# Kernel optimization log

Measured on AMD Instinct MI355X. Metric: run time of the kernel, lower is better.

The kernel has to match this reference:

```python
import jax, jax.numpy as jnp
import numpy as np

N_JOB, N_SKILL = 100000, 20000
H, D = 4, 64            # heads, per-head dim (hidden_channels)
F_DIM = H * D           # 256 = heads * hidden_channels
IN = 256                # in_channels
E_SJ, E_JJ, E_JS = 500000, 500000, 250000


def setup_inputs() -> dict:
    key = jax.random.key(0)
    ks = jax.random.split(key, 24)
    rn = lambda k, s, sc=0.05: jax.random.normal(k, s, dtype=jnp.float32) * sc
    z = lambda s: jnp.zeros(s, jnp.float32)
    return dict(
        x_job=rn(ks[0], (N_JOB, IN), 1.0),
        x_skill=rn(ks[1], (N_SKILL, IN), 1.0),
        W_job=rn(ks[2], (IN, F_DIM)), b_job=z((F_DIM,)),
        W_skill=rn(ks[3], (IN, F_DIM)), b_skill=z((F_DIM,)),
        a_src_sj=rn(ks[4], (H, D)), a_dst_sj=rn(ks[5], (H, D)),
        a_src_jj=rn(ks[6], (H, D)), a_dst_jj=rn(ks[7], (H, D)),
        a_src_js=rn(ks[8], (H, D)), a_dst_js=rn(ks[9], (H, D)),
        q=rn(ks[10], (F_DIM,)), Wk=rn(ks[11], (F_DIM, F_DIM)), bk=z((F_DIM,)),
        W1=rn(ks[12], (F_DIM, F_DIM)), b1=z((F_DIM,)),
        W2=rn(ks[13], (F_DIM, 1)), b2=z((1,)),
        ei_sj_src=jax.random.randint(ks[14], (E_SJ,), 0, N_SKILL),
        ei_sj_dst=jax.random.randint(ks[15], (E_SJ,), 0, N_JOB),
        ei_jj_src=jax.random.randint(ks[16], (E_JJ,), 0, N_JOB),
        ei_jj_dst=jax.random.randint(ks[17], (E_JJ,), 0, N_JOB),
        ei_js_src=jax.random.randint(ks[18], (E_JS,), 0, N_JOB),
        ei_js_dst=jax.random.randint(ks[19], (E_JS,), 0, N_SKILL),
    )


def _gat(x_src, x_dst, a_src, a_dst, src, dst, n_dst):
    # x_src: [Ns,H,D], x_dst: [Nd,H,D]; GAT-style node-level attention per edge type.
    al = jnp.einsum('nhd,hd->nh', x_src, a_src)[src] + jnp.einsum('nhd,hd->nh', x_dst, a_dst)[dst]
    al = jax.nn.leaky_relu(al, 0.2)                      # [E,H]
    amax = jax.lax.stop_gradient(jax.ops.segment_max(al, dst, n_dst))
    e = jnp.exp(al - amax[dst])
    denom = jax.ops.segment_sum(e, dst, n_dst)
    alpha = e / (denom[dst] + 1e-16)                     # softmax over incoming edges per dst
    out = jax.ops.segment_sum(x_src[src] * alpha[:, :, None], dst, n_dst)  # [Nd,H,D]
    return jax.nn.relu(out.reshape(n_dst, H * D))


def _group(outs, q, Wk, bk):
    # semantic-level attention across edge types (shared q, k_lin)
    stk = jnp.stack(outs)                                # [M,N,F]
    score = jnp.einsum('f,mf->m', q, jnp.tanh(stk @ Wk + bk).mean(1))
    attn = jax.nn.softmax(score)
    return jnp.einsum('m,mnf->nf', attn, stk)


def reference(x_job, x_skill, W_job, b_job, W_skill, b_skill,
              a_src_sj, a_dst_sj, a_src_jj, a_dst_jj, a_src_js, a_dst_js,
              q, Wk, bk, W1, b1, W2, b2,
              ei_sj_src, ei_sj_dst, ei_jj_src, ei_jj_dst, ei_js_src, ei_js_dst):
    h_job = (x_job @ W_job + b_job).reshape(N_JOB, H, D)
    h_skill = (x_skill @ W_skill + b_skill).reshape(N_SKILL, H, D)
    out_sj = _gat(h_skill, h_job, a_src_sj, a_dst_sj, ei_sj_src, ei_sj_dst, N_JOB)
    out_jj = _gat(h_job, h_job, a_src_jj, a_dst_jj, ei_jj_src, ei_jj_dst, N_JOB)
    out_js = _gat(h_job, h_skill, a_src_js, a_dst_js, ei_js_src, ei_js_dst, N_SKILL)
    job = _group([out_sj, out_jj], q, Wk, bk)            # 'job' node type
    _ = _group([out_js], q, Wk, bk)                      # 'skill' node type (unused by head)
    # dropout is identity in eval mode; MLP head (mlp_layers=2)
    h = jax.nn.relu(job @ W1 + b1)
    return (h @ W2 + b2)[:, 0]
```

## Files before the change

### kernel.cpp

```cpp
#include <hip/hip_runtime.h>
#include <hip/hip_bf16.h>
#include <math.h>

#define SCAN_B 256
#define NEG_BIG (-3.0e38f)

typedef __attribute__((ext_vector_type(8))) short bf16x8;
typedef __attribute__((ext_vector_type(4))) float f32x4;

__device__ __forceinline__ unsigned short f2bf(float f) {
    __hip_bfloat16 h = __float2bfloat16(f);
    return *(unsigned short*)&h;
}
__device__ __forceinline__ float bf2f(unsigned short u) {
    unsigned v = ((unsigned)u) << 16;
    return __uint_as_float(v);
}
__device__ __forceinline__ float lrelu(float x) { return (x >= 0.f) ? x : 0.2f * x; }

__device__ __forceinline__ unsigned blend2(unsigned a, unsigned b, float c0, float c1) {
    float alo = bf2f((unsigned short)(a & 0xffff)), ahi = bf2f((unsigned short)(a >> 16));
    float blo = bf2f((unsigned short)(b & 0xffff)), bhi = bf2f((unsigned short)(b >> 16));
    unsigned short rlo = f2bf(c0 * alo + c1 * blo);
    unsigned short rhi = f2bf(c0 * ahi + c1 * bhi);
    return (unsigned)rlo | ((unsigned)rhi << 16);
}

__device__ __forceinline__ void fma8(float* a, uint4 u, float w) {
    a[0] += w * __uint_as_float(u.x << 16);
    a[1] += w * __uint_as_float(u.x & 0xffff0000u);
    a[2] += w * __uint_as_float(u.y << 16);
    a[3] += w * __uint_as_float(u.y & 0xffff0000u);
    a[4] += w * __uint_as_float(u.z << 16);
    a[5] += w * __uint_as_float(u.z & 0xffff0000u);
    a[6] += w * __uint_as_float(u.w << 16);
    a[7] += w * __uint_as_float(u.w & 0xffff0000u);
}

template<int MODE, int NV, int AF32>
__launch_bounds__(512)
__global__ void gemm_mfma(const float* __restrict__ Af32,
                          const unsigned short* __restrict__ Abf,
                          const unsigned short* __restrict__ A2bf,
                          const unsigned short* __restrict__ Bt,
                          const float* __restrict__ bias,
                          const float* __restrict__ vq,
                          const float* __restrict__ b2p,
                          const float* __restrict__ attn2,
                          unsigned short* __restrict__ outh,
                          float* __restrict__ outf,
                          float* __restrict__ scoreSlot,
                          const float* __restrict__ av0,
                          const float* __restrict__ av1,
                          const float* __restrict__ av2,
                          float* __restrict__ lo0,
                          float* __restrict__ lo1,
                          float* __restrict__ lo2,
                          int M)
{
    __shared__ __align__(16) char sm[49152];
    __shared__ float red8[8];
    const int t    = threadIdx.x;
    const int lane = t & 63, wid = t >> 6;
    const int wr = wid >> 2, wc = wid & 3;
    const long row0 = (long)blockIdx.x * 128;
    const char* Ab = (const char*)((MODE == 1 && blockIdx.y == 1) ? A2bf : Abf);
    const char* A2 = (const char*)A2bf;
    const char* Bb = (const char*)Bt;

    float blend0 = 0.f, blend1 = 0.f;
    if (MODE == 2) { blend0 = attn2[0]; blend1 = attn2[1]; }

    f32x4 acc[4][4];
#pragma unroll
    for (int m = 0; m < 4; ++m)
#pragma unroll
        for (int n = 0; n < 4; ++n) acc[m][n] = (f32x4){0.f, 0.f, 0.f, 0.f};

    for (int k0 = 0; k0 < 256; k0 += 64) {
#pragma unroll
        for (int rep = 0; rep < 2; ++rep) {
            int idx = rep * 512 + t;
            int row = idx >> 3, colb = (idx & 7) << 4;
            uint4 v;
            if (AF32) {
                long grow = row0 + row;
                if (grow < M) {
                    const float* sp = Af32 + grow * 256 + k0 + ((idx & 7) << 3);
                    float4 f0 = *(const float4*)sp;
                    float4 f1 = *(const float4*)(sp + 4);
                    v.x = (unsigned)f2bf(f0.x) | ((unsigned)f2bf(f0.y) << 16);
                    v.y = (unsigned)f2bf(f0.z) | ((unsigned)f2bf(f0.w) << 16);
                    v.z = (unsigned)f2bf(f1.x) | ((unsigned)f2bf(f1.y) << 16);
                    v.w = (unsigned)f2bf(f1.z) | ((unsigned)f2bf(f1.w) << 16);
                } else {
                    v = make_uint4(0u, 0u, 0u, 0u);
                }
            } else {
                v = *(const uint4*)(Ab + (row0 + row) * 512 + k0 * 2 + colb);
                if (MODE == 2) {
                    uint4 v2 = *(const uint4*)(A2 + (row0 + row) * 512 + k0 * 2 + colb);
                    v.x = blend2(v.x, v2.x, blend0, blend1);
                    v.y = blend2(v.y, v2.y, blend0, blend1);
                    v.z = blend2(v.z, v2.z, blend0, blend1);
                    v.w = blend2(v.w, v2.w, blend0, blend1);
                }
            }
            *(uint4*)&sm[row * 128 + (colb ^ ((row & 7) << 4))] = v;
        }
#pragma unroll
        for (int rep = 0; rep < 4; ++rep) {
            int idx = rep * 512 + t;
            int n = idx >> 3, colb = (idx & 7) << 4;
            uint4 v = *(const uint4*)(Bb + n * 512 + k0 * 2 + colb);
            *(uint4*)&sm[16384 + n * 128 + (colb ^ ((n & 7) << 4))] = v;
        }
        __syncthreads();
#pragma unroll
        for (int kki = 0; kki < 2; ++kki) {
            const int kb = kki * 64 + ((lane >> 4) << 4);
            bf16x8 a[4], b[4];
#pragma unroll
            for (int m = 0; m < 4; ++m) {
                int row = wr * 64 + m * 16 + (lane & 15);
                a[m] = *(const bf16x8*)&sm[row * 128 + (kb ^ ((row & 7) << 4))];
            }
#pragma unroll
            for (int n = 0; n < 4; ++n) {
                int nr = wc * 64 + n * 16 + (lane & 15);
                b[n] = *(const bf16x8*)&sm[16384 + nr * 128 + (kb ^ ((nr & 7) << 4))];
            }
#pragma unroll
            for (int m = 0; m < 4; ++m)
#pragma unroll
                for (int n = 0; n < 4; ++n)
                    acc[m][n] = __builtin_amdgcn_mfma_f32_16x16x32_bf16(a[m], b[n], acc[m][n], 0, 0, 0);
        }
        __syncthreads();
    }

    const int colbase = wc * 64 + (lane & 15);
    const int rbase   = wr * 64 + ((lane >> 4) << 2);
    float bv[4];
#pragma unroll
    for (int n = 0; n < 4; ++n) bv[n] = bias[colbase + n * 16];

    if (MODE == 0) {
        float areg[(NV > 0) ? NV : 1][4];
#pragma unroll
        for (int v = 0; v < NV; ++v) {
            const float* av = (v == 0) ? av0 : (v == 1) ? av1 : av2;
#pragma unroll
            for (int n = 0; n < 4; ++n) areg[v][n] = av[colbase + n * 16];
        }
#pragma unroll
        for (int m = 0; m < 4; ++m) {
#pragma unroll
            for (int j = 0; j < 4; ++j) {
                long row = row0 + rbase + m * 16 + j;
                float hv[4];
#pragma unroll
                for (int n = 0; n < 4; ++n) hv[n] = acc[m][n][j] + bv[n];
                if (row < M) {
#pragma unroll
                    for (int n = 0; n < 4; ++n)
                        outh[row * 256 + colbase + n * 16] = f2bf(hv[n]);
                }
#pragma unroll
                for (int v = 0; v < NV; ++v) {
                    float p = hv[0] * areg[v][0] + hv[1] * areg[v][1]
                            + hv[2] * areg[v][2] + hv[3] * areg[v][3];
                    p += __shfl_xor(p, 1); p += __shfl_xor(p, 2);
                    p += __shfl_xor(p, 4); p += __shfl_xor(p, 8);
                    if ((lane & 15) == 0 && row < M) {
                        float* lo = (v == 0) ? lo0 : (v == 1) ? lo1 : lo2;
                        lo[row * 4 + wc] = p;
                    }
                }
            }
        }
    } else if (MODE == 1) {
        float p = 0.f;
        float qv[4];
#pragma unroll
        for (int n = 0; n < 4; ++n) qv[n] = vq[colbase + n * 16];
#pragma unroll
        for (int n = 0; n < 4; ++n) {
#pragma unroll
            for (int m = 0; m < 4; ++m) {
                long row = row0 + rbase + m * 16;
#pragma unroll
                for (int j = 0; j < 4; ++j)
                    if (row + j < M) p += qv[n] * tanhf(acc[m][n][j] + bv[n]);
            }
        }
#pragma unroll
        for (int off = 32; off > 0; off >>= 1) p += __shfl_xor(p, off);
        if (lane == 0) red8[wid] = p;
        __syncthreads();
        if (t == 0) {
            float s = 0.f;
#pragma unroll
            for (int i = 0; i < 8; ++i) s += red8[i];
            atomicAdd(&scoreSlot[blockIdx.y], s);
        }
    } else {
        float* redC = (float*)sm;
        float b2v = b2p[0];
        float wv[4];
#pragma unroll
        for (int n = 0; n < 4; ++n) wv[n] = vq[colbase + n * 16];
#pragma unroll
        for (int m = 0; m < 4; ++m) {
#pragma unroll
            for (int j = 0; j < 4; ++j) {
                float s = 0.f;
#pragma unroll
                for (int n = 0; n < 4; ++n)
                    s += fmaxf(acc[m][n][j] + bv[n], 0.f) * wv[n];
                s += __shfl_xor(s, 1); s += __shfl_xor(s, 2);
                s += __shfl_xor(s, 4); s += __shfl_xor(s, 8);
                if ((lane & 15) == 0) {
                    int lrow = wr * 64 + m * 16 + ((lane >> 4) << 2) + j;
                    redC[lrow * 4 + wc] = s;
                }
            }
        }
        __syncthreads();
        if (t < 128) {
            long row = row0 + t;
            if (row < M)
                outf[row] = redC[t * 4 + 0] + redC[t * 4 + 1]
                          + redC[t * 4 + 2] + redC[t * 4 + 3] + b2v;
        }
    }
}

__global__ void transpose_cast4(const float* __restrict__ W0, const float* __restrict__ W1s,
                                const float* __restrict__ W2s, const float* __restrict__ W3s,
                                unsigned short* __restrict__ T0, unsigned short* __restrict__ T1,
                                unsigned short* __restrict__ T2, unsigned short* __restrict__ T3)
{
    const float* W = (blockIdx.y == 0) ? W0 : (blockIdx.y == 1) ? W1s : (blockIdx.y == 2) ? W2s : W3s;
    unsigned short* T = (blockIdx.y == 0) ? T0 : (blockIdx.y == 1) ? T1 : (blockIdx.y == 2) ? T2 : T3;
    int n = blockIdx.x, k = threadIdx.x;
    T[n * 256 + k] = f2bf(W[k * 256 + n]);
}

__global__ void hist2(const int* __restrict__ d0, int E0, int* __restrict__ g0,
                      const int* __restrict__ d1, int E1, int* __restrict__ g1)
{
    int e = blockIdx.x * 256 + threadIdx.x;
    if (blockIdx.y == 0) { if (e < E0) atomicAdd(&g0[d0[e]], 1); }
    else                 { if (e < E1) atomicAdd(&g1[d1[e]], 1); }
}

__global__ void scan_bsum2(const int* __restrict__ g0, const int* __restrict__ g1, int n,
                           int* __restrict__ p0, int* __restrict__ p1)
{
    const int* deg = blockIdx.y ? g1 : g0;
    int* part      = blockIdx.y ? p1 : p0;
    __shared__ int smem[SCAN_B];
    int i = blockIdx.x * SCAN_B + threadIdx.x;
    smem[threadIdx.x] = (i < n) ? deg[i] : 0;
    __syncthreads();
    for (int off = SCAN_B / 2; off > 0; off >>= 1) {
        if (threadIdx.x < off) smem[threadIdx.x] += smem[threadIdx.x + off];
        __syncthreads();
    }
    if (threadIdx.x == 0) part[blockIdx.x] = smem[0];
}

__global__ void scan_part2(int* __restrict__ p0, int* __restrict__ p1, int nb)
{
    int* part = blockIdx.y ? p1 : p0;
    __shared__ int smem[1024];
    int t = threadIdx.x;
    int v = (t < nb) ? part[t] : 0;
    smem[t] = v;
    __syncthreads();
    for (int off = 1; off < 1024; off <<= 1) {
        int add = (t >= off) ? smem[t - off] : 0;
        __syncthreads();
        smem[t] += add;
        __syncthreads();
    }
    if (t < nb) part[t] = smem[t] - v;
}

__global__ void scan_final2(const int* __restrict__ g0, const int* __restrict__ g1, int n,
                            const int* __restrict__ p0, const int* __restrict__ p1,
                            int* __restrict__ r0, int* __restrict__ r1, int E0, int E1)
{
    const int* deg = blockIdx.y ? g1 : g0;
    const int* part = blockIdx.y ? p1 : p0;
    int* rowptr = blockIdx.y ? r1 : r0;
    int E = blockIdx.y ? E1 : E0;
    __shared__ int smem[SCAN_B];
    int t = threadIdx.x;
    int i = blockIdx.x * SCAN_B + t;
    int v = (i < n) ? deg[i] : 0;
    smem[t] = v;
    __syncthreads();
    for (int off = 1; off < SCAN_B; off <<= 1) {
        int add = (t >= off) ? smem[t - off] : 0;
        __syncthreads();
        smem[t] += add;
        __syncthreads();
    }
    if (i < n) rowptr[i] = part[blockIdx.x] + smem[t] - v;
    if (blockIdx.x == 0 && t == 0) rowptr[n] = E;
}

__global__ void fill_csr2(const int* __restrict__ d0, int E0, const int* __restrict__ r0,
                          int* __restrict__ c0, int* __restrict__ o0,
                          const int* __restrict__ d1, int E1, const int* __restrict__ r1,
                          int* __restrict__ c1, int* __restrict__ o1)
{
    int e = blockIdx.x * 256 + threadIdx.x;
    if (blockIdx.y == 0) {
        if (e < E0) { int d = d0[e]; int s = atomicAdd(&c0[d], 1); o0[r0[d] + s] = e; }
    } else {
        if (e < E1) { int d = d1[e]; int s = atomicAdd(&c1[d], 1); o1[r1[d] + s] = e; }
    }
}

__launch_bounds__(256)
__global__ void gat_fused(const unsigned short* __restrict__ xs0,
                          const unsigned short* __restrict__ xs1,
                          const float* __restrict__ als0, const float* __restrict__ als1,
                          const float* __restrict__ ald0, const float* __restrict__ ald1,
                          const int* __restrict__ rp0, const int* __restrict__ rp1,
                          const int* __restrict__ csr0, const int* __restrict__ csr1,
                          const int* __restrict__ src0, const int* __restrict__ src1,
                          int N,
                          unsigned short* __restrict__ out0,
                          unsigned short* __restrict__ out1)
{
    const int et = blockIdx.y;
    const unsigned short* xsrc = et ? xs1 : xs0;
    const float* als = et ? als1 : als0;
    const float* ald = et ? ald1 : ald0;
    const int* rowptr = et ? rp1 : rp0;
    const int* csr    = et ? csr1 : csr0;
    const int* src    = et ? src1 : src0;
    unsigned short* outb = et ? out1 : out0;

    __shared__ float lw[4][64 * 4];
    __shared__ int   ls[4][64];
    const int wv   = threadIdx.x >> 6;
    const int w    = (int)((blockIdx.x * 256 + threadIdx.x) >> 6);
    const int lane = threadIdx.x & 63;
    if (w >= N) return;
    const int beg = rowptr[w], end = rowptr[w + 1];
    const int deg = end - beg;
    const int sub = lane & 31, half = lane >> 5;
    const int h2 = sub >> 3;
    const float4 d4 = *(const float4*)&ald[(size_t)w * 4];
    const size_t loff8 = (size_t)(sub << 3);

    float a8A[8] = {0.f, 0.f, 0.f, 0.f, 0.f, 0.f, 0.f, 0.f};
    float a8B[8] = {0.f, 0.f, 0.f, 0.f, 0.f, 0.f, 0.f, 0.f};
    float dn0 = 0.f, dn1 = 0.f, dn2 = 0.f, dn3 = 0.f;

    if (deg <= 64) {
        float al0 = NEG_BIG, al1 = NEG_BIG, al2 = NEG_BIG, al3 = NEG_BIG;
        int es = 0;
        if (lane < deg) {
            int e = csr[beg + lane];
            es = src[e];
            float4 a = *(const float4*)&als[(size_t)es * 4];
            al0 = lrelu(a.x + d4.x); al1 = lrelu(a.y + d4.y);
            al2 = lrelu(a.z + d4.z); al3 = lrelu(a.w + d4.w);
        }
        float m0 = al0, m1 = al1, m2 = al2, m3 = al3;
#pragma unroll
        for (int off = 32; off > 0; off >>= 1) {
            m0 = fmaxf(m0, __shfl_xor(m0, off));
            m1 = fmaxf(m1, __shfl_xor(m1, off));
            m2 = fmaxf(m2, __shfl_xor(m2, off));
            m3 = fmaxf(m3, __shfl_xor(m3, off));
        }
        float w0 = 0.f, w1 = 0.f, w2 = 0.f, w3 = 0.f;
        if (lane < deg) {
            w0 = expf(al0 - m0); w1 = expf(al1 - m1);
            w2 = expf(al2 - m2); w3 = expf(al3 - m3);
            ls[wv][lane] = es;
            lw[wv][lane * 4 + 0] = w0; lw[wv][lane * 4 + 1] = w1;
            lw[wv][lane * 4 + 2] = w2; lw[wv][lane * 4 + 3] = w3;
        }
        dn0 = w0; dn1 = w1; dn2 = w2; dn3 = w3;

        int i = 0;
        for (; i + 4 <= deg; i += 4) {
            int eA = i + half, eB = i + 2 + half;
            int sA = ls[wv][eA], sB = ls[wv][eB];
            float wA = lw[wv][eA * 4 + h2], wB = lw[wv][eB * 4 + h2];
            uint4 xA = *(const uint4*)&xsrc[(size_t)sA * 256 + loff8];
            uint4 xB = *(const uint4*)&xsrc[(size_t)sB * 256 + loff8];
            fma8(a8A, xA, wA);
            fma8(a8B, xB, wB);
        }
        if (i + 2 <= deg) {
            int eA = i + half;
            int sA = ls[wv][eA];
            float wA = lw[wv][eA * 4 + h2];
            uint4 xA = *(const uint4*)&xsrc[(size_t)sA * 256 + loff8];
            fma8(a8A, xA, wA);
            i += 2;
        }
        if (i < deg) {
            int sA = ls[wv][i];
            float wA = half ? 0.f : lw[wv][i * 4 + h2];
            uint4 xA = *(const uint4*)&xsrc[(size_t)sA * 256 + loff8];
            fma8(a8A, xA, wA);
        }
    } else {
        float m0 = NEG_BIG, m1 = NEG_BIG, m2 = NEG_BIG, m3 = NEG_BIG;
        for (int c = beg; c < end; c += 64) {
            if (c + lane < end) {
                int e = csr[c + lane];
                int s = src[e];
                float4 a = *(const float4*)&als[(size_t)s * 4];
                m0 = fmaxf(m0, lrelu(a.x + d4.x)); m1 = fmaxf(m1, lrelu(a.y + d4.y));
                m2 = fmaxf(m2, lrelu(a.z + d4.z)); m3 = fmaxf(m3, lrelu(a.w + d4.w));
            }
        }
#pragma unroll
        for (int off = 32; off > 0; off >>= 1) {
            m0 = fmaxf(m0, __shfl_xor(m0, off));
            m1 = fmaxf(m1, __shfl_xor(m1, off));
            m2 = fmaxf(m2, __shfl_xor(m2, off));
            m3 = fmaxf(m3, __shfl_xor(m3, off));
        }
        for (int c = beg; c < end; c += 64) {
            int cnt = min(64, end - c);
            if (lane < cnt) {
                int e = csr[c + lane];
                int es = src[e];
                float4 a = *(const float4*)&als[(size_t)es * 4];
                float w0 = expf(lrelu(a.x + d4.x) - m0);
                float w1 = expf(lrelu(a.y + d4.y) - m1);
                float w2 = expf(lrelu(a.z + d4.z) - m2);
                float w3 = expf(lrelu(a.w + d4.w) - m3);
                ls[wv][lane] = es;
                lw[wv][lane * 4 + 0] = w0; lw[wv][lane * 4 + 1] = w1;
                lw[wv][lane * 4 + 2] = w2; lw[wv][lane * 4 + 3] = w3;
                dn0 += w0; dn1 += w1; dn2 += w2; dn3 += w3;
            }
            int i = 0;
            for (; i + 4 <= cnt; i += 4) {
                int eA = i + half, eB = i + 2 + half;
                int sA = ls[wv][eA], sB = ls[wv][eB];
                float wA = lw[wv][eA * 4 + h2], wB = lw[wv][eB * 4 + h2];
                uint4 xA = *(const uint4*)&xsrc[(size_t)sA * 256 + loff8];
                uint4 xB = *(const uint4*)&xsrc[(size_t)sB * 256 + loff8];
                fma8(a8A, xA, wA);
                fma8(a8B, xB, wB);
            }
            if (i + 2 <= cnt) {
                int eA = i + half;
                int sA = ls[wv][eA];
                float wA = lw[wv][eA * 4 + h2];
                uint4 xA = *(const uint4*)&xsrc[(size_t)sA * 256 + loff8];
                fma8(a8A, xA, wA);
                i += 2;
            }
            if (i < cnt) {
                int sA = ls[wv][i];
                float wA = half ? 0.f : lw[wv][i * 4 + h2];
                uint4 xA = *(const uint4*)&xsrc[(size_t)sA * 256 + loff8];
                fma8(a8A, xA, wA);
            }
        }
    }

#pragma unroll
    for (int j = 0; j < 8; ++j) a8A[j] += a8B[j];
#pragma unroll
    for (int j = 0; j < 8; ++j) a8A[j] += __shfl_xor(a8A[j], 32);

#pragma unroll
    for (int off = 32; off > 0; off >>= 1) {
        dn0 += __shfl_xor(dn0, off);
        dn1 += __shfl_xor(dn1, off);
        dn2 += __shfl_xor(dn2, off);
        dn3 += __shfl_xor(dn3, off);
    }
    float dh = (h2 == 0) ? dn0 : (h2 == 1) ? dn1 : (h2 == 2) ? dn2 : dn3;
    float inv = 1.f / (dh + 1e-16f);
    if (half == 0) {
        uint4 o;
        o.x = (unsigned)f2bf(fmaxf(a8A[0] * inv, 0.f)) | ((unsigned)f2bf(fmaxf(a8A[1] * inv, 0.f)) << 16);
        o.y = (unsigned)f2bf(fmaxf(a8A[2] * inv, 0.f)) | ((unsigned)f2bf(fmaxf(a8A[3] * inv, 0.f)) << 16);
        o.z = (unsigned)f2bf(fmaxf(a8A[4] * inv, 0.f)) | ((unsigned)f2bf(fmaxf(a8A[5] * inv, 0.f)) << 16);
        o.w = (unsigned)f2bf(fmaxf(a8A[6] * inv, 0.f)) | ((unsigned)f2bf(fmaxf(a8A[7] * inv, 0.f)) << 16);
        *(uint4*)&outb[(size_t)w * 256 + loff8] = o;
    }
}

__global__ void attn_k(const float* __restrict__ score, float* __restrict__ attn, float invN)
{
    if (threadIdx.x == 0 && blockIdx.x == 0) {
        float s0 = score[0] * invN, s1 = score[1] * invN;
        float m  = fmaxf(s0, s1);
        float e0 = expf(s0 - m), e1 = expf(s1 - m);
        float dsum = e0 + e1;
        attn[0] = e0 / dsum;
        attn[1] = e1 / dsum;
    }
}

extern "C" void kernel_launch(void* const* d_in, const int* in_sizes, int n_in,
                              void* d_out, int out_size, void* d_ws, size_t ws_size,
                              hipStream_t stream)
{
    const float* x_job    = (const float*)d_in[0];
    const float* x_skill  = (const float*)d_in[1];
    const float* W_job    = (const float*)d_in[2];
    const float* b_job    = (const float*)d_in[3];
    const float* W_skill  = (const float*)d_in[4];
    const float* b_skill  = (const float*)d_in[5];
    const float* a_src_sj = (const float*)d_in[6];
    const float* a_dst_sj = (const float*)d_in[7];
    const float* a_src_jj = (const float*)d_in[8];
    const float* a_dst_jj = (const float*)d_in[9];
    const float* q_vec = (const float*)d_in[12];
    const float* Wk    = (const float*)d_in[13];
    const float* bk    = (const float*)d_in[14];
    const float* W1    = (const float*)d_in[15];
    const float* b1    = (const float*)d_in[16];
    const float* W2    = (const float*)d_in[17];
    const float* b2    = (const float*)d_in[18];
    const int* ei_sj_src = (const int*)d_in[19];
    const int* ei_sj_dst = (const int*)d_in[20];
    const int* ei_jj_src = (const int*)d_in[21];
    const int* ei_jj_dst = (const int*)d_in[22];

    const int NJ   = in_sizes[0] / 256;
    const int NS   = in_sizes[1] / 256;
    const int E_sj = in_sizes[19];
    const int E_jj = in_sizes[21];
    const int Emax = (E_sj > E_jj) ? E_sj : E_jj;
    const int gmJ  = (NJ + 127) / 128, gmS = (NS + 127) / 128;
    const long MpadJ = (long)gmJ * 128, MpadS = (long)gmS * 128;

    char* ws   = (char*)d_ws;
    size_t off = 0;
    auto alloc = [&](size_t bytes) { void* p = ws + off; off += (bytes + 255) & ~(size_t)255; return p; };
    unsigned short* h_job_bf   = (unsigned short*)alloc(MpadJ * 256 * 2);
    unsigned short* h_skill_bf = (unsigned short*)alloc(MpadS * 256 * 2);
    unsigned short* Wjob_t  = (unsigned short*)alloc(256 * 256 * 2);
    unsigned short* Wskl_t  = (unsigned short*)alloc(256 * 256 * 2);
    unsigned short* Wk_t    = (unsigned short*)alloc(256 * 256 * 2);
    unsigned short* W1_t    = (unsigned short*)alloc(256 * 256 * 2);
    unsigned short* out_sj_bf = (unsigned short*)alloc(MpadJ * 256 * 2);
    unsigned short* out_jj_bf = (unsigned short*)alloc(MpadJ * 256 * 2);
    float* ald_sj  = (float*)alloc((size_t)NJ * 4 * 4);
    float* als_jj  = (float*)alloc((size_t)NJ * 4 * 4);
    float* ald_jj  = (float*)alloc((size_t)NJ * 4 * 4);
    float* als_sj  = (float*)alloc((size_t)NS * 4 * 4);
    float* score  = (float*)alloc(64 * 4);
    float* attn   = score + 2;
    int* deg_sj = (int*)alloc((size_t)NJ * 4);
    int* deg_jj = (int*)alloc((size_t)NJ * 4);
    int* rp_sj  = (int*)alloc(((size_t)NJ + 1) * 4);
    int* rp_jj  = (int*)alloc(((size_t)NJ + 1) * 4);
    int* part_a = (int*)alloc(1024 * 4);
    int* part_b = (int*)alloc(1024 * 4);
    int* cur_sj = (int*)alloc((size_t)NJ * 4);
    int* cur_jj = (int*)alloc((size_t)NJ * 4);
    int* csr_sj = (int*)alloc((size_t)E_sj * 4);
    int* csr_jj = (int*)alloc((size_t)E_jj * 4);
    (void)ws_size; (void)n_in;

    hipMemsetAsync(score,  0, 2 * 4, stream);
    hipMemsetAsync(deg_sj, 0, (size_t)NJ * 4, stream);
    hipMemsetAsync(deg_jj, 0, (size_t)NJ * 4, stream);
    hipMemsetAsync(cur_sj, 0, (size_t)NJ * 4, stream);
    hipMemsetAsync(cur_jj, 0, (size_t)NJ * 4, stream);

    dim3 blk(256);
    int nbJ = (NJ + SCAN_B - 1) / SCAN_B;

    transpose_cast4<<<dim3(256, 4), blk, 0, stream>>>(
        W_job, W_skill, Wk, W1, Wjob_t, Wskl_t, Wk_t, W1_t);

    hist2<<<dim3((Emax + 255) / 256, 2), blk, 0, stream>>>(
        ei_sj_dst, E_sj, deg_sj, ei_jj_dst, E_jj, deg_jj);
    scan_bsum2<<<dim3(nbJ, 2), dim3(SCAN_B), 0, stream>>>(deg_sj, deg_jj, NJ, part_a, part_b);
    scan_part2<<<dim3(1, 2), dim3(1024), 0, stream>>>(part_a, part_b, nbJ);
    scan_final2<<<dim3(nbJ, 2), dim3(SCAN_B), 0, stream>>>(
        deg_sj, deg_jj, NJ, part_a, part_b, rp_sj, rp_jj, E_sj, E_jj);
    fill_csr2<<<dim3((Emax + 255) / 256, 2), blk, 0, stream>>>(
        ei_sj_dst, E_sj, rp_sj, cur_sj, csr_sj,
        ei_jj_dst, E_jj, rp_jj, cur_jj, csr_jj);

    gemm_mfma<0, 3, 1><<<dim3(gmJ), dim3(512), 0, stream>>>(
        x_job, nullptr, nullptr, Wjob_t, b_job, nullptr, nullptr, nullptr,
        h_job_bf, nullptr, nullptr,
        a_dst_sj, a_src_jj, a_dst_jj, ald_sj, als_jj, ald_jj, NJ);
    gemm_mfma<0, 1, 1><<<dim3(gmS), dim3(512), 0, stream>>>(
        x_skill, nullptr, nullptr, Wskl_t, b_skill, nullptr, nullptr, nullptr,
        h_skill_bf, nullptr, nullptr,
        a_src_sj, nullptr, nullptr, als_sj, nullptr, nullptr, NS);

    gat_fused<<<dim3((NJ + 3) / 4, 2), blk, 0, stream>>>(
        h_skill_bf, h_job_bf, als_sj, als_jj, ald_sj, ald_jj,
        rp_sj, rp_jj, csr_sj, csr_jj, ei_sj_src, ei_jj_src, NJ,
        out_sj_bf, out_jj_bf);

    gemm_mfma<1, 0, 0><<<dim3(gmJ, 2), dim3(512), 0, stream>>>(
        nullptr, out_sj_bf, out_jj_bf, Wk_t, bk, q_vec, nullptr, nullptr,
        nullptr, nullptr, score,
        nullptr, nullptr, nullptr, nullptr, nullptr, nullptr, NJ);
    attn_k<<<1, 64, 0, stream>>>(score, attn, 1.0f / (float)NJ);

    gemm_mfma<2, 0, 0><<<dim3(gmJ), dim3(512), 0, stream>>>(
        nullptr, out_sj_bf, out_jj_bf, W1_t, b1, W2, b2, attn,
        nullptr, (float*)d_out, nullptr,
        nullptr, nullptr, nullptr, nullptr, nullptr, nullptr, NJ);
}
```

Baseline: 466.6 us.

## Process both job edge types per wavefront with interleaved 4-wide gathers

Replaces the two-block-row GAT kernel, which gave each edge type its own wavefront, with one kernel where each wavefront handles both sj and jj edges for a destination job. The gather is restructured so each lane covers 4 features (ushort4) of a single edge instead of 8 features across two half-waves, and A and B gathers are interleaved with 4-edge unrolling to keep more independent loads in flight. This halves the wavefront count, removes the cross-half shuffle reduction and doubles per-wave memory-level parallelism, at the cost of smaller 8-byte loads, more LDS and register use per block, and serialising the two edge types inside a single wavefront.

```diff
diff --git a/kernel.cpp b/kernel.cpp
--- a/kernel.cpp
+++ b/kernel.cpp
@@ -26,15 +26,9 @@
     return (unsigned)rlo | ((unsigned)rhi << 16);
 }
 
-__device__ __forceinline__ void fma8(float* a, uint4 u, float w) {
-    a[0] += w * __uint_as_float(u.x << 16);
-    a[1] += w * __uint_as_float(u.x & 0xffff0000u);
-    a[2] += w * __uint_as_float(u.y << 16);
-    a[3] += w * __uint_as_float(u.y & 0xffff0000u);
-    a[4] += w * __uint_as_float(u.z << 16);
-    a[5] += w * __uint_as_float(u.z & 0xffff0000u);
-    a[6] += w * __uint_as_float(u.w << 16);
-    a[7] += w * __uint_as_float(u.w & 0xffff0000u);
+__device__ __forceinline__ void fma4(float* a, ushort4 u, float w) {
+    a[0] += w * bf2f(u.x); a[1] += w * bf2f(u.y);
+    a[2] += w * bf2f(u.z); a[3] += w * bf2f(u.w);
 }
 
 template<int MODE, int NV, int AF32>
@@ -326,50 +320,41 @@
 }
 
 __launch_bounds__(256)
-__global__ void gat_fused(const unsigned short* __restrict__ xs0,
-                          const unsigned short* __restrict__ xs1,
-                          const float* __restrict__ als0, const float* __restrict__ als1,
-                          const float* __restrict__ ald0, const float* __restrict__ ald1,
-                          const int* __restrict__ rp0, const int* __restrict__ rp1,
-                          const int* __restrict__ csr0, const int* __restrict__ csr1,
-                          const int* __restrict__ src0, const int* __restrict__ src1,
-                          int N,
-                          unsigned short* __restrict__ out0,
-                          unsigned short* __restrict__ out1)
-{
-    const int et = blockIdx.y;
-    const unsigned short* xsrc = et ? xs1 : xs0;
-    const float* als = et ? als1 : als0;
-    const float* ald = et ? ald1 : ald0;
-    const int* rowptr = et ? rp1 : rp0;
-    const int* csr    = et ? csr1 : csr0;
-    const int* src    = et ? src1 : src0;
-    unsigned short* outb = et ? out1 : out0;
-
-    __shared__ float lw[4][64 * 4];
-    __shared__ int   ls[4][64];
+__global__ void gat_dual(const unsigned short* __restrict__ xsA,
+                         const unsigned short* __restrict__ xsB,
+                         const float* __restrict__ alsA, const float* __restrict__ alsB,
+                         const float* __restrict__ aldA, const float* __restrict__ aldB,
+                         const int* __restrict__ rpA, const int* __restrict__ rpB,
+                         const int* __restrict__ csrA, const int* __restrict__ csrB,
+                         const int* __restrict__ srcA, const int* __restrict__ srcB,
+                         int N,
+                         unsigned short* __restrict__ outA,
+                         unsigned short* __restrict__ outB)
+{
+    __shared__ float lwA[4][64 * 4], lwB[4][64 * 4];
+    __shared__ int   lsA[4][64],     lsB[4][64];
     const int wv   = threadIdx.x >> 6;
     const int w    = (int)((blockIdx.x * 256 + threadIdx.x) >> 6);
     const int lane = threadIdx.x & 63;
     if (w >= N) return;
-    const int beg = rowptr[w], end = rowptr[w + 1];
-    const int deg = end - beg;
-    const int sub = lane & 31, half = lane >> 5;
-    const int h2 = sub >> 3;
-    const float4 d4 = *(const float4*)&ald[(size_t)w * 4];
-    const size_t loff8 = (size_t)(sub << 3);
-
-    float a8A[8] = {0.f, 0.f, 0.f, 0.f, 0.f, 0.f, 0.f, 0.f};
-    float a8B[8] = {0.f, 0.f, 0.f, 0.f, 0.f, 0.f, 0.f, 0.f};
-    float dn0 = 0.f, dn1 = 0.f, dn2 = 0.f, dn3 = 0.f;
-
-    if (deg <= 64) {
+    const int begA = rpA[w], degA = rpA[w + 1] - begA;
+    const int begB = rpB[w], degB = rpB[w + 1] - begB;
+    const int h = lane >> 4;
+    const size_t loff = (size_t)(lane << 2);
+
+    float accA[4] = {0.f, 0.f, 0.f, 0.f};
+    float accB[4] = {0.f, 0.f, 0.f, 0.f};
+    float dnA[4] = {0.f, 0.f, 0.f, 0.f};
+    float dnB[4] = {0.f, 0.f, 0.f, 0.f};
+
+    if (degA <= 64) {
+        const float4 d4 = *(const float4*)&aldA[(size_t)w * 4];
         float al0 = NEG_BIG, al1 = NEG_BIG, al2 = NEG_BIG, al3 = NEG_BIG;
         int es = 0;
-        if (lane < deg) {
-            int e = csr[beg + lane];
-            es = src[e];
-            float4 a = *(const float4*)&als[(size_t)es * 4];
+        if (lane < degA) {
+            int e = csrA[begA + lane];
+            es = srcA[e];
+            float4 a = *(const float4*)&alsA[(size_t)es * 4];
             al0 = lrelu(a.x + d4.x); al1 = lrelu(a.y + d4.y);
             al2 = lrelu(a.z + d4.z); al3 = lrelu(a.w + d4.w);
         }
@@ -381,51 +366,27 @@
             m2 = fmaxf(m2, __shfl_xor(m2, off));
             m3 = fmaxf(m3, __shfl_xor(m3, off));
         }
-        float w0 = 0.f, w1 = 0.f, w2 = 0.f, w3 = 0.f;
-        if (lane < deg) {
-            w0 = expf(al0 - m0); w1 = expf(al1 - m1);
-            w2 = expf(al2 - m2); w3 = expf(al3 - m3);
-            ls[wv][lane] = es;
-            lw[wv][lane * 4 + 0] = w0; lw[wv][lane * 4 + 1] = w1;
-            lw[wv][lane * 4 + 2] = w2; lw[wv][lane * 4 + 3] = w3;
-        }
-        dn0 = w0; dn1 = w1; dn2 = w2; dn3 = w3;
-
-        int i = 0;
-        for (; i + 4 <= deg; i += 4) {
-            int eA = i + half, eB = i + 2 + half;
-            int sA = ls[wv][eA], sB = ls[wv][eB];
-            float wA = lw[wv][eA * 4 + h2], wB = lw[wv][eB * 4 + h2];
-            uint4 xA = *(const uint4*)&xsrc[(size_t)sA * 256 + loff8];
-            uint4 xB = *(const uint4*)&xsrc[(size_t)sB * 256 + loff8];
-            fma8(a8A, xA, wA);
-            fma8(a8B, xB, wB);
-        }
-        if (i + 2 <= deg) {
-            int eA = i + half;
-            int sA = ls[wv][eA];
-            float wA = lw[wv][eA * 4 + h2];
-            uint4 xA = *(const uint4*)&xsrc[(size_t)sA * 256 + loff8];
-            fma8(a8A, xA, wA);
-            i += 2;
-        }
-        if (i < deg) {
-            int sA = ls[wv][i];
-            float wA = half ? 0.f : lw[wv][i * 4 + h2];
-            uint4 xA = *(const uint4*)&xsrc[(size_t)sA * 256 + loff8];
-            fma8(a8A, xA, wA);
-        }
-    } else {
-        float m0 = NEG_BIG, m1 = NEG_BIG, m2 = NEG_BIG, m3 = NEG_BIG;
-        for (int c = beg; c < end; c += 64) {
-            if (c + lane < end) {
-                int e = csr[c + lane];
-                int s = src[e];
-                float4 a = *(const float4*)&als[(size_t)s * 4];
-                m0 = fmaxf(m0, lrelu(a.x + d4.x)); m1 = fmaxf(m1, lrelu(a.y + d4.y));
-                m2 = fmaxf(m2, lrelu(a.z + d4.z)); m3 = fmaxf(m3, lrelu(a.w + d4.w));
-            }
-        }
+        if (lane < degA) {
+            float w0 = expf(al0 - m0), w1 = expf(al1 - m1);
+            float w2 = expf(al2 - m2), w3 = expf(al3 - m3);
+            lsA[wv][lane] = es;
+            lwA[wv][lane * 4 + 0] = w0; lwA[wv][lane * 4 + 1] = w1;
+            lwA[wv][lane * 4 + 2] = w2; lwA[wv][lane * 4 + 3] = w3;
+            dnA[0] = w0; dnA[1] = w1; dnA[2] = w2; dnA[3] = w3;
+        }
+    }
+    if (degB <= 64) {
+        const float4 d4 = *(const float4*)&aldB[(size_t)w * 4];
+        float al0 = NEG_BIG, al1 = NEG_BIG, al2 = NEG_BIG, al3 = NEG_BIG;
+        int es = 0;
+        if (lane < degB) {
+            int e = csrB[begB + lane];
+            es = srcB[e];
+            float4 a = *(const float4*)&alsB[(size_t)es * 4];
+            al0 = lrelu(a.x + d4.x); al1 = lrelu(a.y + d4.y);
+            al2 = lrelu(a.z + d4.z); al3 = lrelu(a.w + d4.w);
+        }
+        float m0 = al0, m1 = al1, m2 = al2, m3 = al3;
 #pragma unroll
         for (int off = 32; off > 0; off >>= 1) {
             m0 = fmaxf(m0, __shfl_xor(m0, off));
@@ -433,70 +394,177 @@
             m2 = fmaxf(m2, __shfl_xor(m2, off));
             m3 = fmaxf(m3, __shfl_xor(m3, off));
         }
-        for (int c = beg; c < end; c += 64) {
-            int cnt = min(64, end - c);
+        if (lane < degB) {
+            float w0 = expf(al0 - m0), w1 = expf(al1 - m1);
+            float w2 = expf(al2 - m2), w3 = expf(al3 - m3);
+            lsB[wv][lane] = es;
+            lwB[wv][lane * 4 + 0] = w0; lwB[wv][lane * 4 + 1] = w1;
+            lwB[wv][lane * 4 + 2] = w2; lwB[wv][lane * 4 + 3] = w3;
+            dnB[0] = w0; dnB[1] = w1; dnB[2] = w2; dnB[3] = w3;
+        }
+    }
+
+    int i = 0, j = 0;
+    if (degA <= 64 && degB <= 64) {
+        for (; i + 4 <= degA && j + 4 <= degB; i += 4, j += 4) {
+            int a0 = lsA[wv][i+0], a1 = lsA[wv][i+1], a2 = lsA[wv][i+2], a3 = lsA[wv][i+3];
+            int b0 = lsB[wv][j+0], b1 = lsB[wv][j+1], b2 = lsB[wv][j+2], b3 = lsB[wv][j+3];
+            float va0 = lwA[wv][(i+0)*4+h], va1 = lwA[wv][(i+1)*4+h];
+            float va2 = lwA[wv][(i+2)*4+h], va3 = lwA[wv][(i+3)*4+h];
+            float vb0 = lwB[wv][(j+0)*4+h], vb1 = lwB[wv][(j+1)*4+h];
+            float vb2 = lwB[wv][(j+2)*4+h], vb3 = lwB[wv][(j+3)*4+h];
+            ushort4 xa0 = *(const ushort4*)&xsA[(size_t)a0 * 256 + loff];
+            ushort4 xa1 = *(const ushort4*)&xsA[(size_t)a1 * 256 + loff];
+            ushort4 xa2 = *(const ushort4*)&xsA[(size_t)a2 * 256 + loff];
+            ushort4 xa3 = *(const ushort4*)&xsA[(size_t)a3 * 256 + loff];
+            ushort4 xb0 = *(const ushort4*)&xsB[(size_t)b0 * 256 + loff];
+            ushort4 xb1 = *(const ushort4*)&xsB[(size_t)b1 * 256 + loff];
+            ushort4 xb2 = *(const ushort4*)&xsB[(size_t)b2 * 256 + loff];
+            ushort4 xb3 = *(const ushort4*)&xsB[(size_t)b3 * 256 + loff];
+            fma4(accA, xa0, va0); fma4(accB, xb0, vb0);
+            fma4(accA, xa1, va1); fma4(accB, xb1, vb1);
+            fma4(accA, xa2, va2); fma4(accB, xb2, vb2);
+            fma4(accA, xa3, va3); fma4(accB, xb3, vb3);
+        }
+    }
+    if (degA <= 64) {
+        for (; i + 4 <= degA; i += 4) {
+            int a0 = lsA[wv][i+0], a1 = lsA[wv][i+1], a2 = lsA[wv][i+2], a3 = lsA[wv][i+3];
+            float va0 = lwA[wv][(i+0)*4+h], va1 = lwA[wv][(i+1)*4+h];
+            float va2 = lwA[wv][(i+2)*4+h], va3 = lwA[wv][(i+3)*4+h];
+            ushort4 xa0 = *(const ushort4*)&xsA[(size_t)a0 * 256 + loff];
+            ushort4 xa1 = *(const ushort4*)&xsA[(size_t)a1 * 256 + loff];
+            ushort4 xa2 = *(const ushort4*)&xsA[(size_t)a2 * 256 + loff];
+            ushort4 xa3 = *(const ushort4*)&xsA[(size_t)a3 * 256 + loff];
+            fma4(accA, xa0, va0); fma4(accA, xa1, va1);
+            fma4(accA, xa2, va2); fma4(accA, xa3, va3);
+        }
+        for (; i < degA; ++i) {
+            int s = lsA[wv][i];
+            float wx = lwA[wv][i * 4 + h];
+            ushort4 xu = *(const ushort4*)&xsA[(size_t)s * 256 + loff];
+            fma4(accA, xu, wx);
+        }
+    } else {
+        const float4 d4 = *(const float4*)&aldA[(size_t)w * 4];
+        float m0 = NEG_BIG, m1 = NEG_BIG, m2 = NEG_BIG, m3 = NEG_BIG;
+        for (int c = 0; c < degA; c += 64) {
+            if (c + lane < degA) {
+                int e = csrA[begA + c + lane];
+                int s = srcA[e];
+                float4 a = *(const float4*)&alsA[(size_t)s * 4];
+                m0 = fmaxf(m0, lrelu(a.x + d4.x)); m1 = fmaxf(m1, lrelu(a.y + d4.y));
+                m2 = fmaxf(m2, lrelu(a.z + d4.z)); m3 = fmaxf(m3, lrelu(a.w + d4.w));
+            }
+        }
+#pragma unroll
+        for (int off = 32; off > 0; off >>= 1) {
+            m0 = fmaxf(m0, __shfl_xor(m0, off));
+            m1 = fmaxf(m1, __shfl_xor(m1, off));
+            m2 = fmaxf(m2, __shfl_xor(m2, off));
+            m3 = fmaxf(m3, __shfl_xor(m3, off));
+        }
+        for (int c = 0; c < degA; c += 64) {
+            int cnt = min(64, degA - c);
             if (lane < cnt) {
-                int e = csr[c + lane];
-                int es = src[e];
-                float4 a = *(const float4*)&als[(size_t)es * 4];
+                int e = csrA[begA + c + lane];
+                int es = srcA[e];
+                float4 a = *(const float4*)&alsA[(size_t)es * 4];
                 float w0 = expf(lrelu(a.x + d4.x) - m0);
                 float w1 = expf(lrelu(a.y + d4.y) - m1);
                 float w2 = expf(lrelu(a.z + d4.z) - m2);
                 float w3 = expf(lrelu(a.w + d4.w) - m3);
-                ls[wv][lane] = es;
-                lw[wv][lane * 4 + 0] = w0; lw[wv][lane * 4 + 1] = w1;
-                lw[wv][lane * 4 + 2] = w2; lw[wv][lane * 4 + 3] = w3;
-                dn0 += w0; dn1 += w1; dn2 += w2; dn3 += w3;
-            }
-            int i = 0;
-            for (; i + 4 <= cnt; i += 4) {
-                int eA = i + half, eB = i + 2 + half;
-                int sA = ls[wv][eA], sB = ls[wv][eB];
-                float wA = lw[wv][eA * 4 + h2], wB = lw[wv][eB * 4 + h2];
-                uint4 xA = *(const uint4*)&xsrc[(size_t)sA * 256 + loff8];
-                uint4 xB = *(const uint4*)&xsrc[(size_t)sB * 256 + loff8];
-                fma8(a8A, xA, wA);
-                fma8(a8B, xB, wB);
-            }
-            if (i + 2 <= cnt) {
-                int eA = i + half;
-                int sA = ls[wv][eA];
-                float wA = lw[wv][eA * 4 + h2];
-                uint4 xA = *(const uint4*)&xsrc[(size_t)sA * 256 + loff8];
-                fma8(a8A, xA, wA);
-                i += 2;
-            }
-            if (i < cnt) {
-                int sA = ls[wv][i];
-                float wA = half ? 0.f : lw[wv][i * 4 + h2];
-                uint4 xA = *(const uint4*)&xsrc[(size_t)sA * 256 + loff8];
-                fma8(a8A, xA, wA);
-            }
-        }
-    }
-
-#pragma unroll
-    for (int j = 0; j < 8; ++j) a8A[j] += a8B[j];
-#pragma unroll
-    for (int j = 0; j < 8; ++j) a8A[j] += __shfl_xor(a8A[j], 32);
+                lsA[wv][lane] = es;
+                lwA[wv][lane * 4 + 0] = w0; lwA[wv][lane * 4 + 1] = w1;
+                lwA[wv][lane * 4 + 2] = w2; lwA[wv][lane * 4 + 3] = w3;
+                dnA[0] += w0; dnA[1] += w1; dnA[2] += w2; dnA[3] += w3;
+            }
+            for (int k = 0; k < cnt; ++k) {
+                int s = lsA[wv][k];
+                float wx = lwA[wv][k * 4 + h];
+                ushort4 xu = *(const ushort4*)&xsA[(size_t)s * 256 + loff];
+                fma4(accA, xu, wx);
+            }
+        }
+    }
+    if (degB <= 64) {
+        for (; j + 4 <= degB; j += 4) {
+            int b0 = lsB[wv][j+0], b1 = lsB[wv][j+1], b2 = lsB[wv][j+2], b3 = lsB[wv][j+3];
+            float vb0 = lwB[wv][(j+0)*4+h], vb1 = lwB[wv][(j+1)*4+h];
+            float vb2 = lwB[wv][(j+2)*4+h], vb3 = lwB[wv][(j+3)*4+h];
+            ushort4 xb0 = *(const ushort4*)&xsB[(size_t)b0 * 256 + loff];
+            ushort4 xb1 = *(const ushort4*)&xsB[(size_t)b1 * 256 + loff];
+            ushort4 xb2 = *(const ushort4*)&xsB[(size_t)b2 * 256 + loff];
+            ushort4 xb3 = *(const ushort4*)&xsB[(size_t)b3 * 256 + loff];
+            fma4(accB, xb0, vb0); fma4(accB, xb1, vb1);
+            fma4(accB, xb2, vb2); fma4(accB, xb3, vb3);
+        }
+        for (; j < degB; ++j) {
+            int s = lsB[wv][j];
+            float wx = lwB[wv][j * 4 + h];
+            ushort4 xu = *(const ushort4*)&xsB[(size_t)s * 256 + loff];
+            fma4(accB, xu, wx);
+        }
+    } else {
+        const float4 d4 = *(const float4*)&aldB[(size_t)w * 4];
+        float m0 = NEG_BIG, m1 = NEG_BIG, m2 = NEG_BIG, m3 = NEG_BIG;
+        for (int c = 0; c < degB; c += 64) {
+            if (c + lane < degB) {
+                int e = csrB[begB + c + lane];
+                int s = srcB[e];
+                float4 a = *(const float4*)&alsB[(size_t)s * 4];
+                m0 = fmaxf(m0, lrelu(a.x + d4.x)); m1 = fmaxf(m1, lrelu(a.y + d4.y));
+                m2 = fmaxf(m2, lrelu(a.z + d4.z)); m3 = fmaxf(m3, lrelu(a.w + d4.w));
+            }
+        }
+#pragma unroll
+        for (int off = 32; off > 0; off >>= 1) {
+            m0 = fmaxf(m0, __shfl_xor(m0, off));
+            m1 = fmaxf(m1, __shfl_xor(m1, off));
+            m2 = fmaxf(m2, __shfl_xor(m2, off));
+            m3 = fmaxf(m3, __shfl_xor(m3, off));
+        }
+        for (int c = 0; c < degB; c += 64) {
+            int cnt = min(64, degB - c);
+            if (lane < cnt) {
+                int e = csrB[begB + c + lane];
+                int es = srcB[e];
+                float4 a = *(const float4*)&alsB[(size_t)es * 4];
+                float w0 = expf(lrelu(a.x + d4.x) - m0);
+                float w1 = expf(lrelu(a.y + d4.y) - m1);
+                float w2 = expf(lrelu(a.z + d4.z) - m2);
+                float w3 = expf(lrelu(a.w + d4.w) - m3);
+                lsB[wv][lane] = es;
+                lwB[wv][lane * 4 + 0] = w0; lwB[wv][lane * 4 + 1] = w1;
+                lwB[wv][lane * 4 + 2] = w2; lwB[wv][lane * 4 + 3] = w3;
+                dnB[0] += w0; dnB[1] += w1; dnB[2] += w2; dnB[3] += w3;
+            }
+            for (int k = 0; k < cnt; ++k) {
+                int s = lsB[wv][k];
+                float wx = lwB[wv][k * 4 + h];
+                ushort4 xu = *(const ushort4*)&xsB[(size_t)s * 256 + loff];
+                fma4(accB, xu, wx);
+            }
+        }
+    }
 
 #pragma unroll
     for (int off = 32; off > 0; off >>= 1) {
-        dn0 += __shfl_xor(dn0, off);
-        dn1 += __shfl_xor(dn1, off);
-        dn2 += __shfl_xor(dn2, off);
-        dn3 += __shfl_xor(dn3, off);
-    }
-    float dh = (h2 == 0) ? dn0 : (h2 == 1) ? dn1 : (h2 == 2) ? dn2 : dn3;
-    float inv = 1.f / (dh + 1e-16f);
-    if (half == 0) {
-        uint4 o;
-        o.x = (unsigned)f2bf(fmaxf(a8A[0] * inv, 0.f)) | ((unsigned)f2bf(fmaxf(a8A[1] * inv, 0.f)) << 16);
-        o.y = (unsigned)f2bf(fmaxf(a8A[2] * inv, 0.f)) | ((unsigned)f2bf(fmaxf(a8A[3] * inv, 0.f)) << 16);
-        o.z = (unsigned)f2bf(fmaxf(a8A[4] * inv, 0.f)) | ((unsigned)f2bf(fmaxf(a8A[5] * inv, 0.f)) << 16);
-        o.w = (unsigned)f2bf(fmaxf(a8A[6] * inv, 0.f)) | ((unsigned)f2bf(fmaxf(a8A[7] * inv, 0.f)) << 16);
-        *(uint4*)&outb[(size_t)w * 256 + loff8] = o;
-    }
+#pragma unroll
+        for (int q = 0; q < 4; ++q) {
+            dnA[q] += __shfl_xor(dnA[q], off);
+            dnB[q] += __shfl_xor(dnB[q], off);
+        }
+    }
+    float invA = 1.f / (dnA[h] + 1e-16f);
+    float invB = 1.f / (dnB[h] + 1e-16f);
+    ushort4 oA, oB;
+    oA.x = f2bf(fmaxf(accA[0] * invA, 0.f)); oA.y = f2bf(fmaxf(accA[1] * invA, 0.f));
+    oA.z = f2bf(fmaxf(accA[2] * invA, 0.f)); oA.w = f2bf(fmaxf(accA[3] * invA, 0.f));
+    oB.x = f2bf(fmaxf(accB[0] * invB, 0.f)); oB.y = f2bf(fmaxf(accB[1] * invB, 0.f));
+    oB.z = f2bf(fmaxf(accB[2] * invB, 0.f)); oB.w = f2bf(fmaxf(accB[3] * invB, 0.f));
+    *(ushort4*)&outA[(size_t)w * 256 + loff] = oA;
+    *(ushort4*)&outB[(size_t)w * 256 + loff] = oB;
 }
 
 __global__ void attn_k(const float* __restrict__ score, float* __restrict__ attn, float invN)
@@ -605,7 +673,7 @@
         h_skill_bf, nullptr, nullptr,
         a_src_sj, nullptr, nullptr, als_sj, nullptr, nullptr, NS);
 
-    gat_fused<<<dim3((NJ + 3) / 4, 2), blk, 0, stream>>>(
+    gat_dual<<<dim3((NJ + 3) / 4), blk, 0, stream>>>(
         h_skill_bf, h_job_bf, als_sj, als_jj, ald_sj, ald_jj,
         rp_sj, rp_jj, csr_sj, csr_jj, ei_sj_src, ei_jj_src, NJ,
         out_sj_bf, out_jj_bf);
```

Measured after the change: 500.3 us. 1.07x slower.
